# Optimization experiments

Hardware: AMD Instinct MI355X
Metric: run time of the kernel (lower is better)

Reference implementation:

```python
import jax, jax.numpy as jnp
import numpy as np
from jax import lax

N, E, T, D = 50000, 400000, 16, 240
HID = 16  # LSTM hidden


def _p(k, shape):
    fan_in = shape[0]
    return jax.random.normal(k, shape, dtype=jnp.float32) * (1.0 / np.sqrt(fan_in))


def setup_inputs() -> dict:
    key = jax.random.key(0)
    ks = jax.random.split(key, 32)
    inp = {
        "x": jax.random.normal(ks[0], (N, D), dtype=jnp.float32),
        "edge_seq": jax.random.normal(ks[1], (E, T, 2), dtype=jnp.float32),
        "node_seq": jax.random.normal(ks[2], (N, T, 2), dtype=jnp.float32),
        # LSTM (torch gate order i,f,g,o); same lstm_edge is used for both edge and node seqs (as in source)
        "lstm_Wih": _p(ks[3], (4 * HID, 2)),
        "lstm_Whh": _p(ks[4], (4 * HID, HID)),
        "lstm_b": jnp.zeros((4 * HID,), jnp.float32),
        "dnn_W": _p(ks[5], (HID, 1)),
        "dnn_b": jnp.zeros((1,), jnp.float32),
        # gat1: in=256, heads=8, out=8 ; gat2: in=64, heads=1, out=64
        "gat1_W": _p(ks[6], (256, 64)),
        "gat1_att": _p(ks[7], (8, 8)),
        "gat1_b": jnp.zeros((64,), jnp.float32),
        "gat2_W": _p(ks[8], (64, 64)),
        "gat2_att": _p(ks[9], (1, 64)),
        "gat2_b": jnp.zeros((64,), jnp.float32),
        "gcn1_W": _p(ks[10], (256, 64)),
        "gcn1_b": jnp.zeros((64,), jnp.float32),
        "gcn2_W": _p(ks[11], (64, 64)),
        "gcn2_b": jnp.zeros((64,), jnp.float32),
        "cls1_W": _p(ks[12], (320, 32)),
        "cls1_b": jnp.zeros((32,), jnp.float32),
        "cls2_W": _p(ks[13], (32, 16)),
        "cls2_b": jnp.zeros((16,), jnp.float32),
        "cls3_W": _p(ks[14], (16, 4)),
        "cls3_b": jnp.zeros((4,), jnp.float32),
        "edge_index": jax.random.randint(ks[15], (2, E), 0, N),
        "edge_len": jax.random.randint(ks[16], (E,), 1, T + 1).astype(jnp.int32),
        "node_len": jax.random.randint(ks[17], (N,), 1, T + 1).astype(jnp.int32),
    }
    return inp


def lstm_last(seq, lens, Wih, Whh, b):
    """Run LSTM over padded [B,T,2] and return hidden at step len-1 (pack/pad_packed semantics)."""
    B, Tt, _ = seq.shape
    H = Whh.shape[1]

    def step(carry, inp):
        h, c, last = carry
        xt, t = inp
        g = xt @ Wih.T + h @ Whh.T + b
        i, f, gg, o = jnp.split(g, 4, axis=-1)
        c = jax.nn.sigmoid(f) * c + jax.nn.sigmoid(i) * jnp.tanh(gg)
        h = jax.nn.sigmoid(o) * jnp.tanh(c)
        last = jnp.where((t == lens - 1)[:, None], h, last)
        return (h, c, last), None

    z = jnp.zeros((B, H), seq.dtype)
    (_, _, last), _ = lax.scan(step, (z, z, z), (jnp.swapaxes(seq, 0, 1), jnp.arange(Tt)))
    return last


def gat_conv(x, src, dst, edge_scalar, W, att, bias, H, C):
    """myGATConv: gather -> leaky_relu -> softmax over dst neighborhoods -> (alpha + edge_mat)*x_j -> scatter-add + residual."""
    n = x.shape[0]
    xh = (x @ W).reshape(n, H, C)                       # [N,H,C]
    alpha = (xh * att[None]).sum(-1)                    # [N,H]
    a = jax.nn.leaky_relu(alpha[src], 0.2)              # [E,H] (alpha_j)
    amax = jax.ops.segment_max(a, dst, num_segments=n)
    ex = jnp.exp(a - amax[dst])
    att_e = ex / jax.ops.segment_sum(ex, dst, num_segments=n)[dst]
    coef = att_e + edge_scalar                          # [E,H] + [E,1] edge bias (edge_mat repeat over heads)
    msg = xh[src] * coef[..., None]                     # [E,H,C]
    out = jax.ops.segment_sum(msg, dst, num_segments=n) + xh  # aggregate + residual
    return out.reshape(n, H * C) + bias


def gcn_conv(x, src, dst, W, b):
    n = x.shape[0]
    xw = x @ W
    deg = jax.ops.segment_sum(jnp.ones(src.shape[0], xw.dtype), dst, num_segments=n) + 1.0  # +self-loop
    dinv = lax.rsqrt(deg)
    norm = (dinv[src] * dinv[dst])[:, None]
    out = jax.ops.segment_sum(xw[src] * norm, dst, num_segments=n) + xw * (dinv * dinv)[:, None]
    return out + b


def reference(x, edge_seq, node_seq, lstm_Wih, lstm_Whh, lstm_b, dnn_W, dnn_b,
              gat1_W, gat1_att, gat1_b, gat2_W, gat2_att, gat2_b,
              gcn1_W, gcn1_b, gcn2_W, gcn2_b,
              cls1_W, cls1_b, cls2_W, cls2_b, cls3_W, cls3_b,
              edge_index, edge_len, node_len):
    src, dst = edge_index[0], edge_index[1]
    # temporal edge branch -> per-edge scalar bias
    edge_feat = lstm_last(edge_seq, edge_len, lstm_Wih, lstm_Whh, lstm_b)   # [E,16]
    edge_scalar = edge_feat @ dnn_W + dnn_b                                 # [E,1]
    # temporal node branch (source reuses lstm_edge) -> concat to node features
    node_feat = lstm_last(node_seq, node_len, lstm_Wih, lstm_Whh, lstm_b)   # [N,16]
    xin = jnp.concatenate([x, node_feat], axis=-1)                          # [N,256]
    # GAT stack (no dropout: eval mode)
    x_gat = gat_conv(xin, src, dst, edge_scalar, gat1_W, gat1_att, gat1_b, 8, 8)
    x_gat = gat_conv(x_gat, src, dst, edge_scalar, gat2_W, gat2_att, gat2_b, 1, 64)
    x_gat = jnp.where(jnp.isinf(x_gat) | jnp.isnan(x_gat), 0.0, x_gat)
    lr = lambda v: jax.nn.leaky_relu(v, 0.01)
    # GCN stack (eval: dropout off)
    x_gcn = lr(gcn_conv(xin, src, dst, gcn1_W, gcn1_b))
    x_gcn = lr(gcn_conv(x_gcn, src, dst, gcn2_W, gcn2_b))
    # classifier head
    h = jnp.concatenate([xin, x_gcn], axis=1)
    h = lr(h @ cls1_W + cls1_b)
    h = lr(h @ cls2_W + cls2_b)
    out = h @ cls3_W + cls3_b
    return (out, x_gcn, x_gat)
```

## Files before the change

### kernel.cpp

```cpp
#include <hip/hip_runtime.h>
#include <hip/hip_bf16.h>


typedef unsigned int u32;

#define NN 50000
#define EE 400000

__device__ float g_nodeF[NN * 16];
__device__ float g_esc[EE];
__device__ float g_P1[NN * 64];
__device__ float g_P2[NN * 64];
__device__ float g_P3[NN * 64];
__device__ float g_P4[NN * 64];
__device__ float g_alpha[NN * 8];
__device__ float g_dinv[NN];
__device__ int   g_cnt[NN];
__device__ int   g_rs[NN + 1];
__device__ int   g_cur[NN];
__device__ int   g_csrc[EE];
__device__ float g_cesc[EE];
__device__ int   g_bhist[32];
__device__ int   g_bbase[32];
__device__ int   g_permN[NN];
__device__ int   g_permE[EE];
__device__ int   g_bsum[256];

__device__ __forceinline__ float rcpf(float x) { return __builtin_amdgcn_rcpf(x); }
__device__ __forceinline__ float sigf(float x) { return rcpf(1.0f + __expf(-x)); }
__device__ __forceinline__ float tanh_fast(float x) {
    return 1.0f - 2.0f * rcpf(__expf(2.0f * x) + 1.0f);
}

typedef short short8 __attribute__((ext_vector_type(8)));
typedef float f32x16 __attribute__((ext_vector_type(16)));

union S8U { short8 v; unsigned u[4]; };

__device__ __forceinline__ unsigned pk_hi(float a, float b) {
    return (__float_as_uint(a) >> 16) | (__float_as_uint(b) & 0xFFFF0000u);
}
__device__ __forceinline__ float bftrunc(float a) {
    return __uint_as_float(__float_as_uint(a) & 0xFFFF0000u);
}
__device__ __forceinline__ float lo_res(float a) { return a - bftrunc(a); }
__device__ __forceinline__ unsigned sx32(unsigned v) {
    return (unsigned)__shfl_xor((int)v, 32, 64);
}

__global__ void __launch_bounds__(256) bucket_hist_kernel(
    const int* __restrict__ nlen, const int* __restrict__ elen,
    const int* __restrict__ dstp, int* __restrict__ cnt)
{
    __shared__ int hb[32];
    int t = threadIdx.x;
    if (t < 32) hb[t] = 0;
    __syncthreads();
    int i = blockIdx.x * 256 + t;
    int bin = -1;
    if (i < NN + EE) {
        bin = (i < NN) ? (16 - nlen[i]) : (32 - elen[i - NN]);
    }
    if (bin >= 0) atomicAdd(&hb[bin], 1);
    if (i < EE) atomicAdd(&cnt[dstp[i]], 1);
    __syncthreads();
    if (t < 32 && hb[t] > 0) atomicAdd(&g_bhist[t], hb[t]);
}

__global__ void __launch_bounds__(64) bucket_scan_kernel()
{
    if (threadIdx.x == 0) {
        int acc = 0;
        for (int b = 0; b < 16; ++b) { g_bbase[b] = acc; acc += g_bhist[b]; }
        acc = 0;
        for (int b = 16; b < 32; ++b) { g_bbase[b] = acc; acc += g_bhist[b]; }
    }
}

__global__ void __launch_bounds__(256) bucket_scatter_kernel(
    const int* __restrict__ nlen, const int* __restrict__ elen)
{
    __shared__ int hb[32];
    int t = threadIdx.x;
    if (t < 32) hb[t] = 0;
    __syncthreads();
    int i = blockIdx.x * 256 + t;
    int bin = -1, idx = 0;
    if (i < NN + EE) {
        if (i < NN) { idx = i; bin = 16 - nlen[i]; }
        else        { idx = i - NN; bin = 32 - elen[i - NN]; }
    }
    if (bin >= 0) atomicAdd(&hb[bin], 1);
    __syncthreads();
    if (t < 32) {
        int c = hb[t];
        hb[t] = c > 0 ? atomicAdd(&g_bbase[t], c) : 0;
    }
    __syncthreads();
    if (bin >= 0) {
        int pos = atomicAdd(&hb[bin], 1);
        if (i < NN) g_permN[pos] = idx; else g_permE[pos] = idx;
    }
}

__global__ void __launch_bounds__(256, 3) lstm_fused_kernel(
    const float* __restrict__ nseq, const int* __restrict__ nlen,
    const float* __restrict__ eseq, const int* __restrict__ elen,
    const float* __restrict__ Wih, const float* __restrict__ Whh,
    const float* __restrict__ bias,
    const float* __restrict__ dnnW, const float* __restrict__ dnnb,
    const int* __restrict__ permN, const int* __restrict__ permE,
    float* __restrict__ nodeF, float* __restrict__ esc, int nNodeBlk)
{
    const int lane = threadIdx.x & 63;
    const int col  = lane & 31;
    const int hi   = lane >> 5;
    const bool isLo = (hi == 0);
    const int wave = threadIdx.x >> 6;

    const bool edgeMode = (int)blockIdx.x >= nNodeBlk;
    const float* seq = edgeMode ? eseq : nseq;
    const int*  lens = edgeMode ? elen : nlen;
    const int*  perm = edgeMode ? permE : permN;
    const int limit  = edgeMode ? EE : NN;
    const int bbase  = edgeMode ? ((int)blockIdx.x - nNodeBlk) : (int)blockIdx.x;
    const int g  = bbase * 128 + wave * 32 + col;
    const int gc = g < limit ? g : limit - 1;
    const int s  = perm[gc];
    const bool valid = g < limit;

    const int row0 = col, row1 = col + 32;
    const int ko = hi * 8;
    S8U ahh0, ahh1, ahl0, ahl1, ax0, ax1;
    {
        const float* w0 = Whh + row0 * 16 + ko;
        const float* w1 = Whh + row1 * 16 + ko;
#pragma unroll
        for (int r = 0; r < 4; ++r) {
            float a0 = w0[2 * r], b0 = w0[2 * r + 1];
            float a1 = w1[2 * r], b1 = w1[2 * r + 1];
            ahh0.u[r] = pk_hi(a0, b0);
            ahh1.u[r] = pk_hi(a1, b1);
            ahl0.u[r] = pk_hi(lo_res(a0), lo_res(b0));
            ahl1.u[r] = pk_hi(lo_res(a1), lo_res(b1));
        }
#pragma unroll
        for (int r = 0; r < 4; ++r) { ax0.u[r] = 0u; ax1.u[r] = 0u; }
        if (isLo) {
            float wa0 = Wih[row0 * 2], wb0 = Wih[row0 * 2 + 1], bb0 = bias[row0];
            float wa1 = Wih[row1 * 2], wb1 = Wih[row1 * 2 + 1], bb1 = bias[row1];
            ax0.u[0] = pk_hi(wa0, wb0);
            ax0.u[1] = pk_hi(bb0, wa0);
            ax0.u[2] = pk_hi(wb0, lo_res(wa0));
            ax0.u[3] = pk_hi(lo_res(wb0), lo_res(bb0));
            ax1.u[0] = pk_hi(wa1, wb1);
            ax1.u[1] = pk_hi(bb1, wa1);
            ax1.u[2] = pk_hi(wb1, lo_res(wa1));
            ax1.u[3] = pk_hi(lo_res(wb1), lo_res(bb1));
        }
    }

    const f32x16 zc = {0.f, 0.f, 0.f, 0.f, 0.f, 0.f, 0.f, 0.f,
                       0.f, 0.f, 0.f, 0.f, 0.f, 0.f, 0.f, 0.f};
    const unsigned bxmask = isLo ? 0xFFFFFFFFu : 0u;
    const unsigned one_bf = 0x3F80u;

    float cst[8], hlast[8];
#pragma unroll
    for (int j = 0; j < 8; ++j) { cst[j] = 0.f; hlast[j] = 0.f; }
    unsigned ph[4], pl[4];
#pragma unroll
    for (int r = 0; r < 4; ++r) { ph[r] = 0u; pl[r] = 0u; }

    const float4* sp = (const float4*)seq + (size_t)s * 8;
    const int lenm1 = lens[s] - 1;
    int lm = lenm1;
#pragma unroll
    for (int off = 32; off >= 1; off >>= 1) {
        int o = __shfl_xor(lm, off, 64);
        lm = lm > o ? lm : o;
    }
    const int nIter = (lm >> 1) + 1;

    float4 q = sp[0];
#pragma unroll 1
    for (int i = 0; i < nIter; ++i) {
        float4 qn = sp[(i + 1) & 7];
#pragma unroll
        for (int hf = 0; hf < 2; ++hf) {
            const int t = 2 * i + hf;
            const float x0 = hf ? q.z : q.x;
            const float x1 = hf ? q.w : q.y;

            S8U bhh, bhl, bx;
            {
                unsigned t0 = sx32(ph[0]), t1 = sx32(ph[1]);
                unsigned t2 = sx32(ph[2]), t3 = sx32(ph[3]);
                bhh.u[0] = isLo ? ph[0] : t2;
                bhh.u[1] = isLo ? ph[1] : t3;
                bhh.u[2] = isLo ? t0 : ph[2];
                bhh.u[3] = isLo ? t1 : ph[3];
                unsigned s0 = sx32(pl[0]), s1 = sx32(pl[1]);
                unsigned s2 = sx32(pl[2]), s3 = sx32(pl[3]);
                bhl.u[0] = isLo ? pl[0] : s2;
                bhl.u[1] = isLo ? pl[1] : s3;
                bhl.u[2] = isLo ? s0 : pl[2];
                bhl.u[3] = isLo ? s1 : pl[3];
            }
            {
                float xl0 = lo_res(x0), xl1 = lo_res(x1);
                bx.u[0] = pk_hi(x0, x1) & bxmask;
                bx.u[1] = (one_bf | (__float_as_uint(xl0) & 0xFFFF0000u)) & bxmask;
                bx.u[2] = pk_hi(xl1, x0) & bxmask;
                bx.u[3] = ((__float_as_uint(x1) >> 16) | (one_bf << 16)) & bxmask;
            }

            f32x16 d0 = __builtin_amdgcn_mfma_f32_32x32x16_bf16(ax0.v, bx.v, zc, 0, 0, 0);
            f32x16 d1 = __builtin_amdgcn_mfma_f32_32x32x16_bf16(ax1.v, bx.v, zc, 0, 0, 0);
            d0 = __builtin_amdgcn_mfma_f32_32x32x16_bf16(ahh0.v, bhh.v, d0, 0, 0, 0);
            d1 = __builtin_amdgcn_mfma_f32_32x32x16_bf16(ahh1.v, bhh.v, d1, 0, 0, 0);
            d0 = __builtin_amdgcn_mfma_f32_32x32x16_bf16(ahl0.v, bhh.v, d0, 0, 0, 0);
            d1 = __builtin_amdgcn_mfma_f32_32x32x16_bf16(ahl1.v, bhh.v, d1, 0, 0, 0);
            d0 = __builtin_amdgcn_mfma_f32_32x32x16_bf16(ahh0.v, bhl.v, d0, 0, 0, 0);
            d1 = __builtin_amdgcn_mfma_f32_32x32x16_bf16(ahh1.v, bhl.v, d1, 0, 0, 0);

            float hh[8];
#pragma unroll
            for (int j = 0; j < 8; ++j) {
                float ip = d0[j], fp = d0[8 + j], gp = d1[j], op = d1[8 + j];
                float cu = sigf(fp) * cst[j] + sigf(ip) * tanh_fast(gp);
                cst[j] = cu;
                hh[j] = sigf(op) * tanh_fast(cu);
            }
            const bool selm = (t == lenm1);
#pragma unroll
            for (int j = 0; j < 8; ++j) hlast[j] = selm ? hh[j] : hlast[j];
#pragma unroll
            for (int r = 0; r < 4; ++r) {
                float a = hh[2 * r], b = hh[2 * r + 1];
                ph[r] = pk_hi(a, b);
                pl[r] = pk_hi(lo_res(a), lo_res(b));
            }
        }
        q = qn;
    }

    if (edgeMode) {
        float4 dA = *(const float4*)(dnnW + hi * 4);
        float4 dB = *(const float4*)(dnnW + hi * 4 + 8);
        float part = hlast[0] * dA.x + hlast[1] * dA.y + hlast[2] * dA.z + hlast[3] * dA.w
                   + hlast[4] * dB.x + hlast[5] * dB.y + hlast[6] * dB.z + hlast[7] * dB.w;
        float tot = part + __shfl_xor(part, 32, 64);
        if (isLo && valid) esc[s] = tot + dnnb[0];
    } else {
        if (valid) {
            float* dst = nodeF + (size_t)s * 16 + hi * 4;
            *(float4*)(dst)     = make_float4(hlast[0], hlast[1], hlast[2], hlast[3]);
            *(float4*)(dst + 8) = make_float4(hlast[4], hlast[5], hlast[6], hlast[7]);
        }
    }
}

__global__ void __launch_bounds__(256) zero_cnt_kernel(int* cnt, int n)
{
    int t = blockIdx.x * 256 + threadIdx.x;
    if (t < n) cnt[t] = 0;
    if (blockIdx.x == 0 && threadIdx.x < 32) g_bhist[threadIdx.x] = 0;
}

__global__ void __launch_bounds__(256) scan1_kernel(const int* __restrict__ cnt, int n)
{
    __shared__ int s[256];
    int t = threadIdx.x;
    int i = blockIdx.x * 256 + t;
    s[t] = (i < n) ? cnt[i] : 0;
    __syncthreads();
#pragma unroll
    for (int off = 128; off >= 1; off >>= 1) {
        if (t < off) s[t] += s[t + off];
        __syncthreads();
    }
    if (t == 0) g_bsum[blockIdx.x] = s[0];
}

__global__ void __launch_bounds__(256) scan3_kernel(
    const int* __restrict__ cnt, int* __restrict__ rs, int* __restrict__ cur,
    float* __restrict__ dinv, int n, int E, int nb)
{
    __shared__ int sb[256];
    __shared__ int s[256];
    int t = threadIdx.x;
    sb[t] = (t < nb) ? g_bsum[t] : 0;
    __syncthreads();
#pragma unroll
    for (int off = 1; off < 256; off <<= 1) {
        int add = (t >= off) ? sb[t - off] : 0;
        __syncthreads();
        sb[t] += add;
        __syncthreads();
    }
    const int boff = (blockIdx.x == 0) ? 0 : sb[blockIdx.x - 1];

    int i = blockIdx.x * 256 + t;
    int v = (i < n) ? cnt[i] : 0;
    s[t] = v;
    __syncthreads();
#pragma unroll
    for (int off = 1; off < 256; off <<= 1) {
        int add = (t >= off) ? s[t - off] : 0;
        __syncthreads();
        s[t] += add;
        __syncthreads();
    }
    if (i < n) {
        int excl = s[t] - v + boff;
        rs[i] = excl;
        cur[i] = excl;
        dinv[i] = rsqrtf((float)v + 1.0f);
    }
    if (i == 0) rs[n] = E;
}

__global__ void __launch_bounds__(256) fill_kernel(const int* __restrict__ src,
                                                   const int* __restrict__ dst,
                                                   const float* __restrict__ esc,
                                                   int* __restrict__ cur,
                                                   int* __restrict__ csrc,
                                                   float* __restrict__ cesc, int E)
{
    int e = blockIdx.x * 256 + threadIdx.x;
    if (e >= E) return;
    int pos = atomicAdd(&cur[dst[e]], 1);
    csrc[pos] = src[e];
    cesc[pos] = esc[e];
}

__global__ void __launch_bounds__(256, 2) gemmX_mfma_kernel(
    const float* __restrict__ x, const float* __restrict__ nodeF,
    const float* __restrict__ W, float* __restrict__ C, int n)
{
    __shared__ unsigned sWhi[128 * 64];
    __shared__ unsigned sWlo[128 * 64];
    const int tid = threadIdx.x;
    for (int i = tid; i < 128 * 64; i += 256) {
        const int kk2 = i >> 6, c = i & 63;
        float a = W[kk2 * 128 + c];
        float b = W[kk2 * 128 + 64 + c];
        sWhi[i] = pk_hi(a, b);
        sWlo[i] = pk_hi(lo_res(a), lo_res(b));
    }
    __syncthreads();

    const int lane = tid & 63;
    const int col  = lane & 31;
    const int hi   = lane >> 5;
    const int wv   = tid >> 6;
    const int nodeBase = blockIdx.x * 128 + wv * 32;
    const int nodeL = nodeBase + col;
    const int nc = nodeL < n ? nodeL : n - 1;

    const f32x16 zc = {0.f, 0.f, 0.f, 0.f, 0.f, 0.f, 0.f, 0.f,
                       0.f, 0.f, 0.f, 0.f, 0.f, 0.f, 0.f, 0.f};
    f32x16 acc0 = zc, acc1 = zc;
    const float* xrow = x + (size_t)nc * 240;
    const float* frow = nodeF + (size_t)nc * 16;

#pragma unroll 1
    for (int ch = 0; ch < 16; ++ch) {
        const float* src = (ch < 15) ? (xrow + ch * 16 + hi * 8) : (frow + hi * 8);
        float4 v0 = *(const float4*)src;
        float4 v1 = *(const float4*)(src + 4);
        S8U xh, xl;
        xh.u[0] = pk_hi(v0.x, v0.y);
        xh.u[1] = pk_hi(v0.z, v0.w);
        xh.u[2] = pk_hi(v1.x, v1.y);
        xh.u[3] = pk_hi(v1.z, v1.w);
        xl.u[0] = pk_hi(lo_res(v0.x), lo_res(v0.y));
        xl.u[1] = pk_hi(lo_res(v0.z), lo_res(v0.w));
        xl.u[2] = pk_hi(lo_res(v1.x), lo_res(v1.y));
        xl.u[3] = pk_hi(lo_res(v1.z), lo_res(v1.w));

        const int rbase = (ch * 8 + hi * 4) * 64 + col;
        S8U wh0, wl0, wh1, wl1;
#pragma unroll
        for (int r = 0; r < 4; ++r) {
            wh0.u[r] = sWhi[rbase + r * 64];
            wl0.u[r] = sWlo[rbase + r * 64];
            wh1.u[r] = sWhi[rbase + r * 64 + 32];
            wl1.u[r] = sWlo[rbase + r * 64 + 32];
        }
        acc0 = __builtin_amdgcn_mfma_f32_32x32x16_bf16(xh.v, wh0.v, acc0, 0, 0, 0);
        acc1 = __builtin_amdgcn_mfma_f32_32x32x16_bf16(xh.v, wh1.v, acc1, 0, 0, 0);
        acc0 = __builtin_amdgcn_mfma_f32_32x32x16_bf16(xl.v, wh0.v, acc0, 0, 0, 0);
        acc1 = __builtin_amdgcn_mfma_f32_32x32x16_bf16(xl.v, wh1.v, acc1, 0, 0, 0);
        acc0 = __builtin_amdgcn_mfma_f32_32x32x16_bf16(xh.v, wl0.v, acc0, 0, 0, 0);
        acc1 = __builtin_amdgcn_mfma_f32_32x32x16_bf16(xh.v, wl1.v, acc1, 0, 0, 0);
    }

#pragma unroll
    for (int r = 0; r < 16; ++r) {
        const int nr = (r & 3) + 8 * (r >> 2) + 4 * hi;
        const int nd = nodeBase + nr;
        if (nd < n) {
            C[(size_t)nd * 64 + col]      = acc0[r];
            C[(size_t)nd * 64 + 32 + col] = acc1[r];
        }
    }
}

__global__ void __launch_bounds__(256, 2) gemm64_mfma_kernel(
    const float* __restrict__ A, const float* __restrict__ W,
    float* __restrict__ C, int n)
{
    __shared__ unsigned sWhi[32 * 64];
    __shared__ unsigned sWlo[32 * 64];
    const int tid = threadIdx.x;
    for (int i = tid; i < 32 * 64; i += 256) {
        const int kk2 = i >> 6, c = i & 63;
        float a = W[kk2 * 128 + c];
        float b = W[kk2 * 128 + 64 + c];
        sWhi[i] = pk_hi(a, b);
        sWlo[i] = pk_hi(lo_res(a), lo_res(b));
    }
    __syncthreads();

    const int lane = tid & 63;
    const int col  = lane & 31;
    const int hi   = lane >> 5;
    const int wv   = tid >> 6;
    const int nodeBase = blockIdx.x * 128 + wv * 32;
    const int nodeL = nodeBase + col;
    const int nc = nodeL < n ? nodeL : n - 1;

    const f32x16 zc = {0.f, 0.f, 0.f, 0.f, 0.f, 0.f, 0.f, 0.f,
                       0.f, 0.f, 0.f, 0.f, 0.f, 0.f, 0.f, 0.f};
    f32x16 acc0 = zc, acc1 = zc;
    const float* arow = A + (size_t)nc * 64;

#pragma unroll
    for (int ch = 0; ch < 4; ++ch) {
        const float* src = arow + ch * 16 + hi * 8;
        float4 v0 = *(const float4*)src;
        float4 v1 = *(const float4*)(src + 4);
        S8U xh, xl;
        xh.u[0] = pk_hi(v0.x, v0.y);
        xh.u[1] = pk_hi(v0.z, v0.w);
        xh.u[2] = pk_hi(v1.x, v1.y);
        xh.u[3] = pk_hi(v1.z, v1.w);
        xl.u[0] = pk_hi(lo_res(v0.x), lo_res(v0.y));
        xl.u[1] = pk_hi(lo_res(v0.z), lo_res(v0.w));
        xl.u[2] = pk_hi(lo_res(v1.x), lo_res(v1.y));
        xl.u[3] = pk_hi(lo_res(v1.z), lo_res(v1.w));

        const int rbase = (ch * 8 + hi * 4) * 64 + col;
        S8U wh0, wl0, wh1, wl1;
#pragma unroll
        for (int r = 0; r < 4; ++r) {
            wh0.u[r] = sWhi[rbase + r * 64];
            wl0.u[r] = sWlo[rbase + r * 64];
            wh1.u[r] = sWhi[rbase + r * 64 + 32];
            wl1.u[r] = sWlo[rbase + r * 64 + 32];
        }
        acc0 = __builtin_amdgcn_mfma_f32_32x32x16_bf16(xh.v, wh0.v, acc0, 0, 0, 0);
        acc1 = __builtin_amdgcn_mfma_f32_32x32x16_bf16(xh.v, wh1.v, acc1, 0, 0, 0);
        acc0 = __builtin_amdgcn_mfma_f32_32x32x16_bf16(xl.v, wh0.v, acc0, 0, 0, 0);
        acc1 = __builtin_amdgcn_mfma_f32_32x32x16_bf16(xl.v, wh1.v, acc1, 0, 0, 0);
        acc0 = __builtin_amdgcn_mfma_f32_32x32x16_bf16(xh.v, wl0.v, acc0, 0, 0, 0);
        acc1 = __builtin_amdgcn_mfma_f32_32x32x16_bf16(xh.v, wl1.v, acc1, 0, 0, 0);
    }

#pragma unroll
    for (int r = 0; r < 16; ++r) {
        const int nr = (r & 3) + 8 * (r >> 2) + 4 * hi;
        const int nd = nodeBase + nr;
        if (nd < n) {
            C[(size_t)nd * 64 + col]      = acc0[r];
            C[(size_t)nd * 64 + 32 + col] = acc1[r];
        }
    }
}

template <int H, int C>
__global__ void __launch_bounds__(256) alpha_kernel(const float* __restrict__ xh,
                                                    const float* __restrict__ att,
                                                    float* __restrict__ alpha, int n)
{
    int t = blockIdx.x * 256 + threadIdx.x;
    if (t >= n * H) return;
    int h = (H == 1) ? 0 : (t % H);
    int nd = (H == 1) ? t : (t / H);
    const float* row = xh + (size_t)nd * 64 + h * C;
    float s = 0.f;
#pragma unroll
    for (int c = 0; c < C; ++c) s += row[c] * att[h * C + c];
    alpha[t] = s;
}

template <int H, bool FILTER>
__global__ void __launch_bounds__(256) fused_gather_kernel(
    const int* __restrict__ rs, const int* __restrict__ csrc,
    const float* __restrict__ cesc, const float* __restrict__ alpha,
    const float* __restrict__ xh, const float* __restrict__ xw,
    const float* __restrict__ dinv,
    const float* __restrict__ gbias, const float* __restrict__ cbias,
    float* __restrict__ gout, float* __restrict__ cout, int n)
{
    const int j = threadIdx.x & 63;
    const int d = blockIdx.x * 4 + (threadIdx.x >> 6);
    if (d >= n) return;
    const int k0 = rs[d], k1 = rs[d + 1];

    float m = -INFINITY, ssum = 0.f;
    if (H == 8) {
        const int e = j >> 3, h = j & 7;
        const int nb = (k1 - k0 + 7) >> 3;
        for (int b = 0; b < nb; ++b) {
            int k = k0 + b * 8 + e;
            if (k < k1) {
                float a = alpha[(size_t)csrc[k] * 8 + h];
                a = a > 0.f ? a : 0.2f * a;
                float mn = fmaxf(m, a);
                ssum = ssum * __expf(m - mn) + __expf(a - mn);
                m = mn;
            }
        }
#pragma unroll
        for (int msk = 8; msk <= 32; msk <<= 1) {
            float mo = __shfl_xor(m, msk, 64);
            float so = __shfl_xor(ssum, msk, 64);
            float mn = fmaxf(m, mo);
            float f1 = (m == -INFINITY) ? 0.f : __expf(m - mn);
            float f2 = (mo == -INFINITY) ? 0.f : __expf(mo - mn);
            ssum = ssum * f1 + so * f2;
            m = mn;
        }
    } else {
        const int nb = (k1 - k0 + 63) >> 6;
        for (int b = 0; b < nb; ++b) {
            int k = k0 + b * 64 + j;
            if (k < k1) {
                float a = alpha[csrc[k]];
                a = a > 0.f ? a : 0.2f * a;
                float mn = fmaxf(m, a);
                ssum = ssum * __expf(m - mn) + __expf(a - mn);
                m = mn;
            }
        }
#pragma unroll
        for (int msk = 1; msk <= 32; msk <<= 1) {
            float mo = __shfl_xor(m, msk, 64);
            float so = __shfl_xor(ssum, msk, 64);
            float mn = fmaxf(m, mo);
            float f1 = (m == -INFINITY) ? 0.f : __expf(m - mn);
            float f2 = (mo == -INFINITY) ? 0.f : __expf(mo - mn);
            ssum = ssum * f1 + so * f2;
            m = mn;
        }
    }
    const int h2 = (H == 8) ? (j >> 3) : 0;
    float mh, ri;
    if (H == 8) {
        mh = __shfl(m, h2, 64);
        ri = rcpf(__shfl(ssum, h2, 64));
    } else {
        mh = m;
        ri = rcpf(ssum);
    }

    const float di = dinv[d];
    float ag = xh[(size_t)d * 64 + j] + gbias[j];
    float ac = xw[(size_t)d * 64 + j] * di * di + cbias[j];
#pragma unroll 2
    for (int k = k0; k < k1; ++k) {
        int s = csrc[k];
        float a = alpha[(size_t)s * H + h2];
        a = a > 0.f ? a : 0.2f * a;
        float coef = __expf(a - mh) * ri + cesc[k];
        ag += xh[(size_t)s * 64 + j] * coef;
        ac += xw[(size_t)s * 64 + j] * (dinv[s] * di);
    }
    if (FILTER && !__builtin_isfinite(ag)) ag = 0.f;
    gout[(size_t)d * 64 + j] = ag;
    cout[(size_t)d * 64 + j] = ac > 0.f ? ac : 0.01f * ac;
}

__global__ void __launch_bounds__(256) cls_kernel(
    const float* __restrict__ x, const float* __restrict__ nodeF,
    const float* __restrict__ xg,
    const float* __restrict__ W1, const float* __restrict__ b1,
    const float* __restrict__ W2, const float* __restrict__ b2,
    const float* __restrict__ W3, const float* __restrict__ b3,
    float* __restrict__ outp, int n)
{
    __shared__ float sW1[320 * 32];
    __shared__ float sW2[32 * 16];
    __shared__ float sW3[16 * 4];
    __shared__ float sb1[32], sb2[16], sb3[4];
    int tid = threadIdx.x;
    for (int i = tid; i < 320 * 32; i += 256) sW1[i] = W1[i];
    for (int i = tid; i < 512; i += 256) sW2[i] = W2[i];
    if (tid < 64) sW3[tid] = W3[tid];
    if (tid < 32) sb1[tid] = b1[tid];
    if (tid < 16) sb2[tid] = b2[tid];
    if (tid < 4)  sb3[tid] = b3[tid];
    __syncthreads();
    int nd = blockIdx.x * 256 + tid;
    if (nd >= n) return;

    float a1[32];
#pragma unroll
    for (int j = 0; j < 32; ++j) a1[j] = sb1[j];
    const float4* xr = (const float4*)(x + (size_t)nd * 240);
#pragma unroll 1
    for (int k4 = 0; k4 < 60; ++k4) {
        float4 v = xr[k4];
        const float* wr = sW1 + k4 * 128;
#pragma unroll
        for (int j = 0; j < 32; ++j)
            a1[j] += v.x * wr[j] + v.y * wr[32 + j] + v.z * wr[64 + j] + v.w * wr[96 + j];
    }
    const float4* nf = (const float4*)(nodeF + (size_t)nd * 16);
#pragma unroll 1
    for (int k4 = 60; k4 < 64; ++k4) {
        float4 v = nf[k4 - 60];
        const float* wr = sW1 + k4 * 128;
#pragma unroll
        for (int j = 0; j < 32; ++j)
            a1[j] += v.x * wr[j] + v.y * wr[32 + j] + v.z * wr[64 + j] + v.w * wr[96 + j];
    }
    const float4* p2 = (const float4*)(xg + (size_t)nd * 64);
#pragma unroll 1
    for (int k4 = 0; k4 < 16; ++k4) {
        float4 v = p2[k4];
        const float* wr = sW1 + 8192 + k4 * 128;
#pragma unroll
        for (int j = 0; j < 32; ++j)
            a1[j] += v.x * wr[j] + v.y * wr[32 + j] + v.z * wr[64 + j] + v.w * wr[96 + j];
    }
#pragma unroll
    for (int j = 0; j < 32; ++j) { float v = a1[j]; a1[j] = v > 0.f ? v : 0.01f * v; }

    float a2[16];
#pragma unroll
    for (int j = 0; j < 16; ++j) a2[j] = sb2[j];
#pragma unroll
    for (int k = 0; k < 32; ++k) {
        float v = a1[k];
        const float* wr = sW2 + k * 16;
#pragma unroll
        for (int j = 0; j < 16; ++j) a2[j] += v * wr[j];
    }
#pragma unroll
    for (int j = 0; j < 16; ++j) { float v = a2[j]; a2[j] = v > 0.f ? v : 0.01f * v; }

    float a3[4] = {sb3[0], sb3[1], sb3[2], sb3[3]};
#pragma unroll
    for (int k = 0; k < 16; ++k) {
        float v = a2[k];
        const float* wr = sW3 + k * 4;
        a3[0] += v * wr[0]; a3[1] += v * wr[1]; a3[2] += v * wr[2]; a3[3] += v * wr[3];
    }
    float4 o = make_float4(a3[0], a3[1], a3[2], a3[3]);
    *(float4*)(outp + (size_t)nd * 4) = o;
}

static inline unsigned nblk(size_t t) { return (unsigned)((t + 255) / 256); }

extern "C" void kernel_launch(void* const* d_in, const int* in_sizes, int n_in,
                              void* d_out, int out_size, void* d_ws, size_t ws_size,
                              hipStream_t stream)
{
    const float* x     = (const float*)d_in[0];
    const float* eseq  = (const float*)d_in[1];
    const float* nseq  = (const float*)d_in[2];
    const float* Wih   = (const float*)d_in[3];
    const float* Whh   = (const float*)d_in[4];
    const float* lb    = (const float*)d_in[5];
    const float* dnnW  = (const float*)d_in[6];
    const float* dnnb  = (const float*)d_in[7];
    const float* g1W   = (const float*)d_in[8];
    const float* g1att = (const float*)d_in[9];
    const float* g1b   = (const float*)d_in[10];
    const float* g2W   = (const float*)d_in[11];
    const float* g2att = (const float*)d_in[12];
    const float* g2b   = (const float*)d_in[13];
    const float* gc1W  = (const float*)d_in[14];
    const float* gc1b  = (const float*)d_in[15];
    const float* gc2W  = (const float*)d_in[16];
    const float* gc2b  = (const float*)d_in[17];
    const float* c1W   = (const float*)d_in[18];
    const float* c1b   = (const float*)d_in[19];
    const float* c2W   = (const float*)d_in[20];
    const float* c2b   = (const float*)d_in[21];
    const float* c3W   = (const float*)d_in[22];
    const float* c3b   = (const float*)d_in[23];
    const int* eidx  = (const int*)d_in[24];
    const int* elen  = (const int*)d_in[25];
    const int* nlen  = (const int*)d_in[26];

    const int N = NN;
    const int E = EE;
    const int* srcp = eidx;
    const int* dstp = eidx + E;

    float *nodeF, *esc, *P1, *P2, *P3, *P4, *alpha, *dinv, *cesc;
    int *cnt, *rs, *cur, *csrc, *permN, *permE;
    hipGetSymbolAddress((void**)&nodeF, HIP_SYMBOL(g_nodeF));
    hipGetSymbolAddress((void**)&esc,   HIP_SYMBOL(g_esc));
    hipGetSymbolAddress((void**)&P1,    HIP_SYMBOL(g_P1));
    hipGetSymbolAddress((void**)&P2,    HIP_SYMBOL(g_P2));
    hipGetSymbolAddress((void**)&P3,    HIP_SYMBOL(g_P3));
    hipGetSymbolAddress((void**)&P4,    HIP_SYMBOL(g_P4));
    hipGetSymbolAddress((void**)&alpha, HIP_SYMBOL(g_alpha));
    hipGetSymbolAddress((void**)&dinv,  HIP_SYMBOL(g_dinv));
    hipGetSymbolAddress((void**)&cnt,   HIP_SYMBOL(g_cnt));
    hipGetSymbolAddress((void**)&rs,    HIP_SYMBOL(g_rs));
    hipGetSymbolAddress((void**)&cur,   HIP_SYMBOL(g_cur));
    hipGetSymbolAddress((void**)&csrc,  HIP_SYMBOL(g_csrc));
    hipGetSymbolAddress((void**)&cesc,  HIP_SYMBOL(g_cesc));
    hipGetSymbolAddress((void**)&permN, HIP_SYMBOL(g_permN));
    hipGetSymbolAddress((void**)&permE, HIP_SYMBOL(g_permE));

    float* out0   = (float*)d_out;
    float* outGcn = out0 + (size_t)N * 4;
    float* outGat = outGcn + (size_t)N * 64;

    zero_cnt_kernel<<<nblk(N), 256, 0, stream>>>(cnt, N);
    bucket_hist_kernel<<<nblk(NN + EE), 256, 0, stream>>>(nlen, elen, dstp, cnt);
    bucket_scan_kernel<<<1, 64, 0, stream>>>();
    bucket_scatter_kernel<<<nblk(NN + EE), 256, 0, stream>>>(nlen, elen);

    const int nNodeBlk = (N + 127) / 128;
    const int nEdgeBlk = (E + 127) / 128;
    lstm_fused_kernel<<<nNodeBlk + nEdgeBlk, 256, 0, stream>>>(
        nseq, nlen, eseq, elen, Wih, Whh, lb, dnnW, dnnb, permN, permE,
        nodeF, esc, nNodeBlk);

    const unsigned scanBlk = nblk(N);
    scan1_kernel<<<scanBlk, 256, 0, stream>>>(cnt, N);
    scan3_kernel<<<scanBlk, 256, 0, stream>>>(cnt, rs, cur, dinv, N, E, (int)scanBlk);
    fill_kernel<<<nblk(E), 256, 0, stream>>>(srcp, dstp, esc, cur, csrc, cesc, E);

    const unsigned gemmBlk = (N + 127) / 128;

    gemmX_mfma_kernel<<<gemmBlk, 256, 0, stream>>>(x, nodeF, g1W, P1, N);
    gemmX_mfma_kernel<<<gemmBlk, 256, 0, stream>>>(x, nodeF, gc1W, P3, N);
    alpha_kernel<8, 8><<<nblk((size_t)N * 8), 256, 0, stream>>>(P1, g1att, alpha, N);
    fused_gather_kernel<8, false><<<(N + 3) / 4, 256, 0, stream>>>(
        rs, csrc, cesc, alpha, P1, P3, dinv, g1b, gc1b, P2, P4, N);

    gemm64_mfma_kernel<<<gemmBlk, 256, 0, stream>>>(P2, g2W, P1, N);
    gemm64_mfma_kernel<<<gemmBlk, 256, 0, stream>>>(P4, gc2W, P3, N);
    alpha_kernel<1, 64><<<nblk(N), 256, 0, stream>>>(P1, g2att, alpha, N);
    fused_gather_kernel<1, true><<<(N + 3) / 4, 256, 0, stream>>>(
        rs, csrc, cesc, alpha, P1, P3, dinv, g2b, gc2b, outGat, outGcn, N);

    cls_kernel<<<nblk(N), 256, 0, stream>>>(x, nodeF, outGcn, c1W, c1b, c2W, c2b, c3W, c3b, out0, N);
}
```

Baseline: 560.9 us.

## Fuse GAT/GCN projection GEMMs with attention logits and prescale LSTM gate weights

```diff
diff --git a/kernel.cpp b/kernel.cpp
--- a/kernel.cpp
+++ b/kernel.cpp
@@ -27,10 +27,8 @@
 __device__ int   g_bsum[256];
 
 __device__ __forceinline__ float rcpf(float x) { return __builtin_amdgcn_rcpf(x); }
+__device__ __forceinline__ float ex2(float x)  { return __builtin_amdgcn_exp2f(x); }
 __device__ __forceinline__ float sigf(float x) { return rcpf(1.0f + __expf(-x)); }
-__device__ __forceinline__ float tanh_fast(float x) {
-    return 1.0f - 2.0f * rcpf(__expf(2.0f * x) + 1.0f);
-}
 
 typedef short short8 __attribute__((ext_vector_type(8)));
 typedef float f32x16 __attribute__((ext_vector_type(16)));
@@ -129,7 +127,10 @@
     const int s  = perm[gc];
     const bool valid = g < limit;
 
+    const float LOG2E = 1.44269504f;
     const int row0 = col, row1 = col + 32;
+    const float s0 = LOG2E;
+    const float s1 = (row1 < 48) ? 2.0f * LOG2E : LOG2E;
     const int ko = hi * 8;
     S8U ahh0, ahh1, ahl0, ahl1, ax0, ax1;
     {
@@ -137,8 +138,8 @@
         const float* w1 = Whh + row1 * 16 + ko;
 #pragma unroll
         for (int r = 0; r < 4; ++r) {
-            float a0 = w0[2 * r], b0 = w0[2 * r + 1];
-            float a1 = w1[2 * r], b1 = w1[2 * r + 1];
+            float a0 = w0[2 * r] * s0, b0 = w0[2 * r + 1] * s0;
+            float a1 = w1[2 * r] * s1, b1 = w1[2 * r + 1] * s1;
             ahh0.u[r] = pk_hi(a0, b0);
             ahh1.u[r] = pk_hi(a1, b1);
             ahl0.u[r] = pk_hi(lo_res(a0), lo_res(b0));
@@ -147,8 +148,8 @@
 #pragma unroll
         for (int r = 0; r < 4; ++r) { ax0.u[r] = 0u; ax1.u[r] = 0u; }
         if (isLo) {
-            float wa0 = Wih[row0 * 2], wb0 = Wih[row0 * 2 + 1], bb0 = bias[row0];
-            float wa1 = Wih[row1 * 2], wb1 = Wih[row1 * 2 + 1], bb1 = bias[row1];
+            float wa0 = Wih[row0 * 2] * s0, wb0 = Wih[row0 * 2 + 1] * s0, bb0 = bias[row0] * s0;
+            float wa1 = Wih[row1 * 2] * s1, wb1 = Wih[row1 * 2 + 1] * s1, bb1 = bias[row1] * s1;
             ax0.u[0] = pk_hi(wa0, wb0);
             ax0.u[1] = pk_hi(bb0, wa0);
             ax0.u[2] = pk_hi(wb0, lo_res(wa0));
@@ -200,12 +201,12 @@
                 bhh.u[1] = isLo ? ph[1] : t3;
                 bhh.u[2] = isLo ? t0 : ph[2];
                 bhh.u[3] = isLo ? t1 : ph[3];
-                unsigned s0 = sx32(pl[0]), s1 = sx32(pl[1]);
-                unsigned s2 = sx32(pl[2]), s3 = sx32(pl[3]);
-                bhl.u[0] = isLo ? pl[0] : s2;
-                bhl.u[1] = isLo ? pl[1] : s3;
-                bhl.u[2] = isLo ? s0 : pl[2];
-                bhl.u[3] = isLo ? s1 : pl[3];
+                unsigned s0u = sx32(pl[0]), s1u = sx32(pl[1]);
+                unsigned s2u = sx32(pl[2]), s3u = sx32(pl[3]);
+                bhl.u[0] = isLo ? pl[0] : s2u;
+                bhl.u[1] = isLo ? pl[1] : s3u;
+                bhl.u[2] = isLo ? s0u : pl[2];
+                bhl.u[3] = isLo ? s1u : pl[3];
             }
             {
                 float xl0 = lo_res(x0), xl1 = lo_res(x1);
@@ -228,9 +229,13 @@
 #pragma unroll
             for (int j = 0; j < 8; ++j) {
                 float ip = d0[j], fp = d0[8 + j], gp = d1[j], op = d1[8 + j];
-                float cu = sigf(fp) * cst[j] + sigf(ip) * tanh_fast(gp);
+                float sig_i = rcpf(1.0f + ex2(-ip));
+                float sig_f = rcpf(1.0f + ex2(-fp));
+                float th_g  = 1.0f - 2.0f * rcpf(ex2(gp) + 1.0f);
+                float cu = sig_f * cst[j] + sig_i * th_g;
                 cst[j] = cu;
-                hh[j] = sigf(op) * tanh_fast(cu);
+                float th_c = 1.0f - 2.0f * rcpf(ex2(cu * 2.88539008f) + 1.0f);
+                hh[j] = rcpf(1.0f + ex2(-op)) * th_c;
             }
             const bool selm = (t == lenm1);
 #pragma unroll
@@ -335,22 +340,15 @@
     cesc[pos] = esc[e];
 }
 
-__global__ void __launch_bounds__(256, 2) gemmX_mfma_kernel(
+__global__ void __launch_bounds__(256, 2) gemmX_dual_kernel(
     const float* __restrict__ x, const float* __restrict__ nodeF,
-    const float* __restrict__ W, float* __restrict__ C, int n)
-{
-    __shared__ unsigned sWhi[128 * 64];
-    __shared__ unsigned sWlo[128 * 64];
+    const float* __restrict__ Wg, const float* __restrict__ Wc,
+    const float* __restrict__ att,
+    float* __restrict__ Pg, float* __restrict__ Pc,
+    float* __restrict__ alpha, int n)
+{
+    __shared__ unsigned sW[2][2][64 * 64];
     const int tid = threadIdx.x;
-    for (int i = tid; i < 128 * 64; i += 256) {
-        const int kk2 = i >> 6, c = i & 63;
-        float a = W[kk2 * 128 + c];
-        float b = W[kk2 * 128 + 64 + c];
-        sWhi[i] = pk_hi(a, b);
-        sWlo[i] = pk_hi(lo_res(a), lo_res(b));
-    }
-    __syncthreads();
-
     const int lane = tid & 63;
     const int col  = lane & 31;
     const int hi   = lane >> 5;
@@ -358,69 +356,113 @@
     const int nodeBase = blockIdx.x * 128 + wv * 32;
     const int nodeL = nodeBase + col;
     const int nc = nodeL < n ? nodeL : n - 1;
+    const float* xrow = x + (size_t)nc * 240;
+    const float* frow = nodeF + (size_t)nc * 16;
+    const float attv0 = att[col];
+    const float attv1 = att[32 + col];
 
     const f32x16 zc = {0.f, 0.f, 0.f, 0.f, 0.f, 0.f, 0.f, 0.f,
                        0.f, 0.f, 0.f, 0.f, 0.f, 0.f, 0.f, 0.f};
-    f32x16 acc0 = zc, acc1 = zc;
-    const float* xrow = x + (size_t)nc * 240;
-    const float* frow = nodeF + (size_t)nc * 16;
+    f32x16 ag0 = zc, ag1 = zc, ac0 = zc, ac1 = zc;
 
 #pragma unroll 1
-    for (int ch = 0; ch < 16; ++ch) {
-        const float* src = (ch < 15) ? (xrow + ch * 16 + hi * 8) : (frow + hi * 8);
-        float4 v0 = *(const float4*)src;
-        float4 v1 = *(const float4*)(src + 4);
-        S8U xh, xl;
-        xh.u[0] = pk_hi(v0.x, v0.y);
-        xh.u[1] = pk_hi(v0.z, v0.w);
-        xh.u[2] = pk_hi(v1.x, v1.y);
-        xh.u[3] = pk_hi(v1.z, v1.w);
-        xl.u[0] = pk_hi(lo_res(v0.x), lo_res(v0.y));
-        xl.u[1] = pk_hi(lo_res(v0.z), lo_res(v0.w));
-        xl.u[2] = pk_hi(lo_res(v1.x), lo_res(v1.y));
-        xl.u[3] = pk_hi(lo_res(v1.z), lo_res(v1.w));
-
-        const int rbase = (ch * 8 + hi * 4) * 64 + col;
-        S8U wh0, wl0, wh1, wl1;
-#pragma unroll
-        for (int r = 0; r < 4; ++r) {
-            wh0.u[r] = sWhi[rbase + r * 64];
-            wl0.u[r] = sWlo[rbase + r * 64];
-            wh1.u[r] = sWhi[rbase + r * 64 + 32];
-            wl1.u[r] = sWlo[rbase + r * 64 + 32];
-        }
-        acc0 = __builtin_amdgcn_mfma_f32_32x32x16_bf16(xh.v, wh0.v, acc0, 0, 0, 0);
-        acc1 = __builtin_amdgcn_mfma_f32_32x32x16_bf16(xh.v, wh1.v, acc1, 0, 0, 0);
-        acc0 = __builtin_amdgcn_mfma_f32_32x32x16_bf16(xl.v, wh0.v, acc0, 0, 0, 0);
-        acc1 = __builtin_amdgcn_mfma_f32_32x32x16_bf16(xl.v, wh1.v, acc1, 0, 0, 0);
-        acc0 = __builtin_amdgcn_mfma_f32_32x32x16_bf16(xh.v, wl0.v, acc0, 0, 0, 0);
-        acc1 = __builtin_amdgcn_mfma_f32_32x32x16_bf16(xh.v, wl1.v, acc1, 0, 0, 0);
+    for (int p = 0; p < 2; ++p) {
+        if (p) __syncthreads();
+        for (int i = tid; i < 2 * 64 * 64; i += 256) {
+            const int mat = i >> 12;
+            const int jj  = i & 4095;
+            const int kk2 = jj >> 6, c = jj & 63;
+            const float* W = mat ? Wc : Wg;
+            float a = W[(p * 64 + kk2) * 128 + c];
+            float b = W[(p * 64 + kk2) * 128 + 64 + c];
+            sW[mat][0][jj] = pk_hi(a, b);
+            sW[mat][1][jj] = pk_hi(lo_res(a), lo_res(b));
+        }
+        __syncthreads();
+#pragma unroll 1
+        for (int ch = 0; ch < 8; ++ch) {
+            const int gch = p * 8 + ch;
+            const float* src = (gch < 15) ? (xrow + gch * 16 + hi * 8) : (frow + hi * 8);
+            float4 v0 = *(const float4*)src;
+            float4 v1 = *(const float4*)(src + 4);
+            S8U xh, xl;
+            xh.u[0] = pk_hi(v0.x, v0.y);
+            xh.u[1] = pk_hi(v0.z, v0.w);
+            xh.u[2] = pk_hi(v1.x, v1.y);
+            xh.u[3] = pk_hi(v1.z, v1.w);
+            xl.u[0] = pk_hi(lo_res(v0.x), lo_res(v0.y));
+            xl.u[1] = pk_hi(lo_res(v0.z), lo_res(v0.w));
+            xl.u[2] = pk_hi(lo_res(v1.x), lo_res(v1.y));
+            xl.u[3] = pk_hi(lo_res(v1.z), lo_res(v1.w));
+
+            const int rbase = (ch * 8 + hi * 4) * 64 + col;
+            S8U gh0, gl0, gh1, gl1, ch0, cl0, ch1, cl1;
+#pragma unroll
+            for (int r = 0; r < 4; ++r) {
+                gh0.u[r] = sW[0][0][rbase + r * 64];
+                gl0.u[r] = sW[0][1][rbase + r * 64];
+                gh1.u[r] = sW[0][0][rbase + r * 64 + 32];
+                gl1.u[r] = sW[0][1][rbase + r * 64 + 32];
+                ch0.u[r] = sW[1][0][rbase + r * 64];
+                cl0.u[r] = sW[1][1][rbase + r * 64];
+                ch1.u[r] = sW[1][0][rbase + r * 64 + 32];
+                cl1.u[r] = sW[1][1][rbase + r * 64 + 32];
+            }
+            ag0 = __builtin_amdgcn_mfma_f32_32x32x16_bf16(xh.v, gh0.v, ag0, 0, 0, 0);
+            ag1 = __builtin_amdgcn_mfma_f32_32x32x16_bf16(xh.v, gh1.v, ag1, 0, 0, 0);
+            ag0 = __builtin_amdgcn_mfma_f32_32x32x16_bf16(xl.v, gh0.v, ag0, 0, 0, 0);
+            ag1 = __builtin_amdgcn_mfma_f32_32x32x16_bf16(xl.v, gh1.v, ag1, 0, 0, 0);
+            ag0 = __builtin_amdgcn_mfma_f32_32x32x16_bf16(xh.v, gl0.v, ag0, 0, 0, 0);
+            ag1 = __builtin_amdgcn_mfma_f32_32x32x16_bf16(xh.v, gl1.v, ag1, 0, 0, 0);
+            ac0 = __builtin_amdgcn_mfma_f32_32x32x16_bf16(xh.v, ch0.v, ac0, 0, 0, 0);
+            ac1 = __builtin_amdgcn_mfma_f32_32x32x16_bf16(xh.v, ch1.v, ac1, 0, 0, 0);
+            ac0 = __builtin_amdgcn_mfma_f32_32x32x16_bf16(xl.v, ch0.v, ac0, 0, 0, 0);
+            ac1 = __builtin_amdgcn_mfma_f32_32x32x16_bf16(xl.v, ch1.v, ac1, 0, 0, 0);
+            ac0 = __builtin_amdgcn_mfma_f32_32x32x16_bf16(xh.v, cl0.v, ac0, 0, 0, 0);
+            ac1 = __builtin_amdgcn_mfma_f32_32x32x16_bf16(xh.v, cl1.v, ac1, 0, 0, 0);
+        }
     }
 
 #pragma unroll
     for (int r = 0; r < 16; ++r) {
         const int nr = (r & 3) + 8 * (r >> 2) + 4 * hi;
         const int nd = nodeBase + nr;
-        if (nd < n) {
-            C[(size_t)nd * 64 + col]      = acc0[r];
-            C[(size_t)nd * 64 + 32 + col] = acc1[r];
-        }
-    }
-}
-
-__global__ void __launch_bounds__(256, 2) gemm64_mfma_kernel(
-    const float* __restrict__ A, const float* __restrict__ W,
-    float* __restrict__ C, int n)
-{
-    __shared__ unsigned sWhi[32 * 64];
-    __shared__ unsigned sWlo[32 * 64];
+        const bool ok = nd < n;
+        if (ok) {
+            Pg[(size_t)nd * 64 + col]      = ag0[r];
+            Pg[(size_t)nd * 64 + 32 + col] = ag1[r];
+            Pc[(size_t)nd * 64 + col]      = ac0[r];
+            Pc[(size_t)nd * 64 + 32 + col] = ac1[r];
+        }
+        float p0 = ag0[r] * attv0;
+        float p1 = ag1[r] * attv1;
+        p0 += __shfl_xor(p0, 1, 64); p0 += __shfl_xor(p0, 2, 64); p0 += __shfl_xor(p0, 4, 64);
+        p1 += __shfl_xor(p1, 1, 64); p1 += __shfl_xor(p1, 2, 64); p1 += __shfl_xor(p1, 4, 64);
+        if (ok && (col & 7) == 0) {
+            alpha[(size_t)nd * 8 + (col >> 3)]     = p0;
+            alpha[(size_t)nd * 8 + 4 + (col >> 3)] = p1;
+        }
+    }
+}
+
+__global__ void __launch_bounds__(256, 2) gemm64_dual_kernel(
+    const float* __restrict__ Ag, const float* __restrict__ Ac,
+    const float* __restrict__ Wg, const float* __restrict__ Wc,
+    const float* __restrict__ att,
+    float* __restrict__ Pg, float* __restrict__ Pc,
+    float* __restrict__ alpha, int n)
+{
+    __shared__ unsigned sW[2][2][32 * 64];
     const int tid = threadIdx.x;
-    for (int i = tid; i < 32 * 64; i += 256) {
-        const int kk2 = i >> 6, c = i & 63;
+    for (int i = tid; i < 2 * 32 * 64; i += 256) {
+        const int mat = i >> 11;
+        const int jj  = i & 2047;
+        const int kk2 = jj >> 6, c = jj & 63;
+        const float* W = mat ? Wc : Wg;
         float a = W[kk2 * 128 + c];
         float b = W[kk2 * 128 + 64 + c];
-        sWhi[i] = pk_hi(a, b);
-        sWlo[i] = pk_hi(lo_res(a), lo_res(b));
+        sW[mat][0][jj] = pk_hi(a, b);
+        sW[mat][1][jj] = pk_hi(lo_res(a), lo_res(b));
     }
     __syncthreads();
 
@@ -431,69 +473,94 @@
     const int nodeBase = blockIdx.x * 128 + wv * 32;
     const int nodeL = nodeBase + col;
     const int nc = nodeL < n ? nodeL : n - 1;
+    const float attv0 = att[col];
+    const float attv1 = att[32 + col];
 
     const f32x16 zc = {0.f, 0.f, 0.f, 0.f, 0.f, 0.f, 0.f, 0.f,
                        0.f, 0.f, 0.f, 0.f, 0.f, 0.f, 0.f, 0.f};
-    f32x16 acc0 = zc, acc1 = zc;
-    const float* arow = A + (size_t)nc * 64;
-
+    f32x16 bg0 = zc, bg1 = zc, bc0 = zc, bc1 = zc;
+
+    const float* garow = Ag + (size_t)nc * 64;
+    const float* carow = Ac + (size_t)nc * 64;
 #pragma unroll
     for (int ch = 0; ch < 4; ++ch) {
-        const float* src = arow + ch * 16 + hi * 8;
-        float4 v0 = *(const float4*)src;
-        float4 v1 = *(const float4*)(src + 4);
-        S8U xh, xl;
-        xh.u[0] = pk_hi(v0.x, v0.y);
-        xh.u[1] = pk_hi(v0.z, v0.w);
-        xh.u[2] = pk_hi(v1.x, v1.y);
-        xh.u[3] = pk_hi(v1.z, v1.w);
-        xl.u[0] = pk_hi(lo_res(v0.x), lo_res(v0.y));
-        xl.u[1] = pk_hi(lo_res(v0.z), lo_res(v0.w));
-        xl.u[2] = pk_hi(lo_res(v1.x), lo_res(v1.y));
-        xl.u[3] = pk_hi(lo_res(v1.z), lo_res(v1.w));
-
         const int rbase = (ch * 8 + hi * 4) * 64 + col;
         S8U wh0, wl0, wh1, wl1;
-#pragma unroll
-        for (int r = 0; r < 4; ++r) {
-            wh0.u[r] = sWhi[rbase + r * 64];
-            wl0.u[r] = sWlo[rbase + r * 64];
-            wh1.u[r] = sWhi[rbase + r * 64 + 32];
-            wl1.u[r] = sWlo[rbase + r * 64 + 32];
-        }
-        acc0 = __builtin_amdgcn_mfma_f32_32x32x16_bf16(xh.v, wh0.v, acc0, 0, 0, 0);
-        acc1 = __builtin_amdgcn_mfma_f32_32x32x16_bf16(xh.v, wh1.v, acc1, 0, 0, 0);
-        acc0 = __builtin_amdgcn_mfma_f32_32x32x16_bf16(xl.v, wh0.v, acc0, 0, 0, 0);
-        acc1 = __builtin_amdgcn_mfma_f32_32x32x16_bf16(xl.v, wh1.v, acc1, 0, 0, 0);
-        acc0 = __builtin_amdgcn_mfma_f32_32x32x16_bf16(xh.v, wl0.v, acc0, 0, 0, 0);
-        acc1 = __builtin_amdgcn_mfma_f32_32x32x16_bf16(xh.v, wl1.v, acc1, 0, 0, 0);
+        {
+            const float* src = garow + ch * 16 + hi * 8;
+            float4 v0 = *(const float4*)src;
+            float4 v1 = *(const float4*)(src + 4);
+            S8U xh, xl;
+            xh.u[0] = pk_hi(v0.x, v0.y);
+            xh.u[1] = pk_hi(v0.z, v0.w);
+            xh.u[2] = pk_hi(v1.x, v1.y);
+            xh.u[3] = pk_hi(v1.z, v1.w);
+            xl.u[0] = pk_hi(lo_res(v0.x), lo_res(v0.y));
+            xl.u[1] = pk_hi(lo_res(v0.z), lo_res(v0.w));
+            xl.u[2] = pk_hi(lo_res(v1.x), lo_res(v1.y));
+            xl.u[3] = pk_hi(lo_res(v1.z), lo_res(v1.w));
+#pragma unroll
+            for (int r = 0; r < 4; ++r) {
+                wh0.u[r] = sW[0][0][rbase + r * 64];
+                wl0.u[r] = sW[0][1][rbase + r * 64];
+                wh1.u[r] = sW[0][0][rbase + r * 64 + 32];
+                wl1.u[r] = sW[0][1][rbase + r * 64 + 32];
+            }
+            bg0 = __builtin_amdgcn_mfma_f32_32x32x16_bf16(xh.v, wh0.v, bg0, 0, 0, 0);
+            bg1 = __builtin_amdgcn_mfma_f32_32x32x16_bf16(xh.v, wh1.v, bg1, 0, 0, 0);
+            bg0 = __builtin_amdgcn_mfma_f32_32x32x16_bf16(xl.v, wh0.v, bg0, 0, 0, 0);
+            bg1 = __builtin_amdgcn_mfma_f32_32x32x16_bf16(xl.v, wh1.v, bg1, 0, 0, 0);
+            bg0 = __builtin_amdgcn_mfma_f32_32x32x16_bf16(xh.v, wl0.v, bg0, 0, 0, 0);
+            bg1 = __builtin_amdgcn_mfma_f32_32x32x16_bf16(xh.v, wl1.v, bg1, 0, 0, 0);
+        }
+        {
+            const float* src = carow + ch * 16 + hi * 8;
+            float4 v0 = *(const float4*)src;
+            float4 v1 = *(const float4*)(src + 4);
+            S8U xh, xl;
+            xh.u[0] = pk_hi(v0.x, v0.y);
+            xh.u[1] = pk_hi(v0.z, v0.w);
+            xh.u[2] = pk_hi(v1.x, v1.y);
+            xh.u[3] = pk_hi(v1.z, v1.w);
+            xl.u[0] = pk_hi(lo_res(v0.x), lo_res(v0.y));
+            xl.u[1] = pk_hi(lo_res(v0.z), lo_res(v0.w));
+            xl.u[2] = pk_hi(lo_res(v1.x), lo_res(v1.y));
+            xl.u[3] = pk_hi(lo_res(v1.z), lo_res(v1.w));
+#pragma unroll
+            for (int r = 0; r < 4; ++r) {
+                wh0.u[r] = sW[1][0][rbase + r * 64];
+                wl0.u[r] = sW[1][1][rbase + r * 64];
+                wh1.u[r] = sW[1][0][rbase + r * 64 + 32];
+                wl1.u[r] = sW[1][1][rbase + r * 64 + 32];
+            }
+            bc0 = __builtin_amdgcn_mfma_f32_32x32x16_bf16(xh.v, wh0.v, bc0, 0, 0, 0);
+            bc1 = __builtin_amdgcn_mfma_f32_32x32x16_bf16(xh.v, wh1.v, bc1, 0, 0, 0);
+            bc0 = __builtin_amdgcn_mfma_f32_32x32x16_bf16(xl.v, wh0.v, bc0, 0, 0, 0);
+            bc1 = __builtin_amdgcn_mfma_f32_32x32x16_bf16(xl.v, wh1.v, bc1, 0, 0, 0);
+            bc0 = __builtin_amdgcn_mfma_f32_32x32x16_bf16(xh.v, wl0.v, bc0, 0, 0, 0);
+            bc1 = __builtin_amdgcn_mfma_f32_32x32x16_bf16(xh.v, wl1.v, bc1, 0, 0, 0);
+        }
     }
 
 #pragma unroll
     for (int r = 0; r < 16; ++r) {
         const int nr = (r & 3) + 8 * (r >> 2) + 4 * hi;
         const int nd = nodeBase + nr;
-        if (nd < n) {
-            C[(size_t)nd * 64 + col]      = acc0[r];
-            C[(size_t)nd * 64 + 32 + col] = acc1[r];
-        }
-    }
-}
-
-template <int H, int C>
-__global__ void __launch_bounds__(256) alpha_kernel(const float* __restrict__ xh,
-                                                    const float* __restrict__ att,
-                                                    float* __restrict__ alpha, int n)
-{
-    int t = blockIdx.x * 256 + threadIdx.x;
-    if (t >= n * H) return;
-    int h = (H == 1) ? 0 : (t % H);
-    int nd = (H == 1) ? t : (t / H);
-    const float* row = xh + (size_t)nd * 64 + h * C;
-    float s = 0.f;
-#pragma unroll
-    for (int c = 0; c < C; ++c) s += row[c] * att[h * C + c];
-    alpha[t] = s;
+        const bool ok = nd < n;
+        if (ok) {
+            Pg[(size_t)nd * 64 + col]      = bg0[r];
+            Pg[(size_t)nd * 64 + 32 + col] = bg1[r];
+            Pc[(size_t)nd * 64 + col]      = bc0[r];
+            Pc[(size_t)nd * 64 + 32 + col] = bc1[r];
+        }
+        float pa = bg0[r] * attv0 + bg1[r] * attv1;
+        pa += __shfl_xor(pa, 1, 64);
+        pa += __shfl_xor(pa, 2, 64);
+        pa += __shfl_xor(pa, 4, 64);
+        pa += __shfl_xor(pa, 8, 64);
+        pa += __shfl_xor(pa, 16, 64);
+        if (ok && col == 0) alpha[nd] = pa;
+    }
 }
 
 template <int H, bool FILTER>
@@ -743,15 +810,13 @@
 
     const unsigned gemmBlk = (N + 127) / 128;
 
-    gemmX_mfma_kernel<<<gemmBlk, 256, 0, stream>>>(x, nodeF, g1W, P1, N);
-    gemmX_mfma_kernel<<<gemmBlk, 256, 0, stream>>>(x, nodeF, gc1W, P3, N);
-    alpha_kernel<8, 8><<<nblk((size_t)N * 8), 256, 0, stream>>>(P1, g1att, alpha, N);
+    gemmX_dual_kernel<<<gemmBlk, 256, 0, stream>>>(
+        x, nodeF, g1W, gc1W, g1att, P1, P3, alpha, N);
     fused_gather_kernel<8, false><<<(N + 3) / 4, 256, 0, stream>>>(
         rs, csrc, cesc, alpha, P1, P3, dinv, g1b, gc1b, P2, P4, N);
 
-    gemm64_mfma_kernel<<<gemmBlk, 256, 0, stream>>>(P2, g2W, P1, N);
-    gemm64_mfma_kernel<<<gemmBlk, 256, 0, stream>>>(P4, gc2W, P3, N);
-    alpha_kernel<1, 64><<<nblk(N), 256, 0, stream>>>(P1, g2att, alpha, N);
+    gemm64_dual_kernel<<<gemmBlk, 256, 0, stream>>>(
+        P2, P4, g2W, gc2W, g2att, P1, P3, alpha, N);
     fused_gather_kernel<1, true><<<(N + 3) / 4, 256, 0, stream>>>(
         rs, csrc, cesc, alpha, P1, P3, dinv, g2b, gc2b, outGat, outGcn, N);
 
```

Measured after the change: 551.4 us. Within noise of the previous version (-1.7%).
